# Kernel tuning notes

Measured on AMD Instinct MI355X. Metric: run time of the kernel, lower is better.

Reference implementation:

```python
import jax, jax.numpy as jnp
import numpy as np

B, L, D, N_NODE = 1024, 32, 128, 50000

def setup_inputs() -> dict:
    key = jax.random.key(0)
    ks = jax.random.split(key, 20)
    rn = lambda k, shape, s=0.05: (jax.random.normal(k, shape, jnp.float32) * s)
    return {
        "items": jax.random.randint(ks[0], (B, L), 0, N_NODE),
        "A_in": jax.random.uniform(ks[1], (B, L, L), jnp.float32),
        "A_out": jax.random.uniform(ks[2], (B, L, L), jnp.float32),
        "inter_item_emb": jax.random.normal(ks[3], (B, L, D), jnp.float32),
        "seq_len": jax.random.randint(ks[4], (B,), 1, L + 1),
        "emb_table": rn(ks[5], (N_NODE, D), 0.1),
        # GGNN propagation weights
        "W_in": rn(ks[6], (D, D)), "b_in": jnp.zeros((D,), jnp.float32),
        "W_out": rn(ks[7], (D, D)), "b_out": jnp.zeros((D,), jnp.float32),
        "W_a": rn(ks[8], (2 * D, 3 * D)),   # acts on concat(a_in, a_out)
        "U_h": rn(ks[9], (D, 3 * D)),       # acts on hidden state
        "b_gru": jnp.zeros((3 * D,), jnp.float32),
        # ItemFusing GRUCell (input=local/intra, hidden=global/inter)
        "Wi": rn(ks[10], (D, 3 * D)), "bi": jnp.zeros((3 * D,), jnp.float32),
        "Wh": rn(ks[11], (D, 3 * D)), "bh": jnp.zeros((3 * D,), jnp.float32),
        # get_final_s attention readout
        "W1": rn(ks[12], (D, D)), "b1": jnp.zeros((D,), jnp.float32),
        "W2": rn(ks[13], (D, D)), "b2": jnp.zeros((D,), jnp.float32),
        "wq": rn(ks[14], (D, 1)), "bq": jnp.zeros((1,), jnp.float32),
        "W3": rn(ks[15], (2 * D, D)), "b3": jnp.zeros((D,), jnp.float32),
    }

def _gru_gates(gi, gh, h_prev):
    # torch GRU(Cell) math: r,z,n gate order
    i_r, i_z, i_n = jnp.split(gi, 3, axis=-1)
    h_r, h_z, h_n = jnp.split(gh, 3, axis=-1)
    r = jax.nn.sigmoid(i_r + h_r)
    z = jax.nn.sigmoid(i_z + h_z)
    n = jnp.tanh(i_n + r * h_n)
    return (1.0 - z) * n + z * h_prev

def reference(items, A_in, A_out, inter_item_emb, seq_len, emb_table,
              W_in, b_in, W_out, b_out, W_a, U_h, b_gru,
              Wi, bi, Wh, bh, W1, b1, W2, b2, wq, bq, W3, b3):
    # --- embedding lookup: [B, L, D]
    h = emb_table[items]
    # --- GGNN propagation (1 step): adjacency matmul + GRU-gated update
    a_in = jnp.einsum('blm,bmd->bld', A_in, h @ W_in + b_in)
    a_out = jnp.einsum('blm,bmd->bld', A_out, h @ W_out + b_out)
    a = jnp.concatenate([a_in, a_out], axis=-1)          # [B, L, 2D]
    intra = _gru_gates(a @ W_a + b_gru, h @ U_h, h)       # [B, L, D]
    # --- ItemFusing: GRUCell(input=intra, hidden=inter)
    final = _gru_gates(intra @ Wi + bi, inter_item_emb @ Wh + bh, inter_item_emb)
    # --- get_final_s (session attention readout, padded/masked form)
    mask = (jnp.arange(L)[None, :] < seq_len[:, None]).astype(final.dtype)  # [B, L]
    v_n = final[jnp.arange(B), seq_len - 1]                                 # [B, D] last valid node
    gates = jax.nn.sigmoid((v_n @ W1 + b1)[:, None, :] + final @ W2 + b2)   # [B, L, D]
    alpha = gates @ wq + bq                                                 # [B, L, 1]
    s_g = jnp.sum(alpha * final * mask[:, :, None], axis=1)                 # [B, D]
    h_s = jnp.concatenate([v_n, s_g], axis=-1) @ W3 + b3                    # [B, D]
    # --- Embedding2Score (item_fusing branch): final_s @ emb.T
    scores = h_s @ emb_table.T                                              # [B, N_NODE]
    return scores
```

## Files before the change

### kernel.cpp

```cpp
#include <hip/hip_runtime.h>
#include <hip/hip_bf16.h>

#define L_SEQ 32
#define DIM 128
#define NN 50000

typedef __attribute__((ext_vector_type(8))) short bf16x8s;
typedef __attribute__((ext_vector_type(4))) float f32x4;

__device__ __forceinline__ float bf2f(short s){
    union{unsigned u; float f;} v; v.u = ((unsigned)(unsigned short)s) << 16; return v.f;
}
__device__ __forceinline__ short f2bf(float x){
    union{__hip_bfloat16 h; short s;} u; u.h = __float2bfloat16(x); return u.s;
}
__device__ __forceinline__ void ldf8(const float* p, float* w){
    const float4 a = *reinterpret_cast<const float4*>(p);
    const float4 b = *reinterpret_cast<const float4*>(p+4);
    w[0]=a.x; w[1]=a.y; w[2]=a.z; w[3]=a.w;
    w[4]=b.x; w[5]=b.y; w[6]=b.z; w[7]=b.w;
}
__device__ __forceinline__ void st8bf(short* dst, const float* v){
    union{ short s[8]; uint4 q; } u;
    #pragma unroll
    for (int i=0;i<8;++i) u.s[i] = f2bf(v[i]);
    *reinterpret_cast<uint4*>(dst) = u.q;
}
__device__ __forceinline__ bf16x8s cvt8(const float* v){
    union{ short s[8]; bf16x8s b; } u;
    #pragma unroll
    for (int i=0;i<8;++i) u.s[i] = f2bf(v[i]);
    return u.b;
}
__device__ __forceinline__ float sigmoidf(float x){ return 1.0f/(1.0f+__expf(-x)); }
__device__ __forceinline__ float tanh_fast(float x){
    x = fminf(fmaxf(x, -15.f), 15.f);
    float e = __expf(2.f*x);
    return (e-1.f)/(e+1.f);
}
__device__ __forceinline__ f32x4 mfma16(bf16x8s a, bf16x8s b, f32x4 c){
    return __builtin_amdgcn_mfma_f32_16x16x32_bf16(a, b, c, 0, 0, 0);
}

__global__ __launch_bounds__(256)
void transp_kernel(const float* __restrict__ W_in, const float* __restrict__ W_out,
                   const float* __restrict__ W_a,  const float* __restrict__ U_h,
                   const float* __restrict__ Wi,   const float* __restrict__ Wh,
                   const float* __restrict__ W1,   const float* __restrict__ W2,
                   const float* __restrict__ W3,   short* __restrict__ wt)
{
    int idx = blockIdx.x*256 + threadIdx.x;
    const float* src; int Rm1, lR, C, local, off;
    if      (idx < 16384) { src=W_in;  local=idx;        off=0;      Rm1=127; lR=7; C=128; }
    else if (idx < 32768) { src=W_out; local=idx-16384;  off=16384;  Rm1=127; lR=7; C=128; }
    else if (idx < 131072){ src=W_a;   local=idx-32768;  off=32768;  Rm1=255; lR=8; C=384; }
    else if (idx < 180224){ src=U_h;   local=idx-131072; off=131072; Rm1=127; lR=7; C=384; }
    else if (idx < 229376){ src=Wi;    local=idx-180224; off=180224; Rm1=127; lR=7; C=384; }
    else if (idx < 278528){ src=Wh;    local=idx-229376; off=229376; Rm1=127; lR=7; C=384; }
    else if (idx < 294912){ src=W1;    local=idx-278528; off=278528; Rm1=127; lR=7; C=128; }
    else if (idx < 311296){ src=W2;    local=idx-294912; off=294912; Rm1=127; lR=7; C=128; }
    else if (idx < 344064){ src=W3;    local=idx-311296; off=311296; Rm1=255; lR=8; C=128; }
    else return;
    int r = local & Rm1;
    int c = local >> lR;
    wt[off + local] = f2bf(src[r*C + c]);
}

__global__ __launch_bounds__(256)
void emb2bf(const float* __restrict__ emb, short* __restrict__ embf)
{
    const size_t idx = (size_t)(blockIdx.x*256 + threadIdx.x) * 8;
    float v[8]; ldf8(emb + idx, v);
    st8bf(embf + idx, v);
}

#define LDH 136
#define LDA 264
#define LDT 40

__global__ __launch_bounds__(256)
void graph_fused(const int* __restrict__ items,
                 const float* __restrict__ A_in, const float* __restrict__ A_out,
                 const float* __restrict__ inter,
                 const int* __restrict__ seq_len,
                 const float* __restrict__ emb,
                 const short* __restrict__ embf,
                 const float* __restrict__ b_in, const float* __restrict__ b_out,
                 const float* __restrict__ b_gru,
                 const float* __restrict__ bi, const float* __restrict__ bh,
                 const float* __restrict__ b1, const float* __restrict__ b2,
                 const float* __restrict__ wq, const float* __restrict__ bq,
                 const float* __restrict__ b3,
                 const short* __restrict__ wt,
                 short* __restrict__ hs_bf)
{
    const short* WinT  = wt + 0;
    const short* WoutT = wt + 16384;
    const short* WaT   = wt + 32768;
    const short* UhT   = wt + 131072;
    const short* WiT   = wt + 180224;
    const short* WhT   = wt + 229376;
    const short* W1T   = wt + 278528;
    const short* W2T   = wt + 294912;
    const short* W3T   = wt + 311296;

    __shared__ __align__(16) short s_h[32*LDH];
    __shared__ __align__(16) short s_a[32*LDA];
    __shared__ __align__(16) short s_r3[32*LDH];
    __shared__ __align__(16) short s_r4[2*32*LDH];

    short* s_Ain  = s_r3;
    short* s_Aout = s_r3 + 32*LDT;
    short* s_x    = s_r3;
    short* xT     = s_r4;
    short* s_int  = s_r4;
    short* s_fin  = s_r4 + 32*LDH;
    float* s_vn    = (float*)s_a;
    float* s_q1    = s_vn + 128;
    float* s_sg    = s_q1 + 128;
    float* s_red   = s_sg + 128;
    float* s_alpha = s_red + 256;

    const int b    = blockIdx.x;
    const int t    = threadIdx.x;
    const int wave = t >> 6;
    const int lane = t & 63;
    const int quad = lane >> 4;
    const int lc   = lane & 15;
    const int kq   = quad * 8;

    if (embf) {
        #pragma unroll
        for (int i=0;i<2;++i) {
            int c = t + i*256;
            int l = c >> 4, k = (c & 15) * 8;
            int it = items[b*L_SEQ + l];
            *reinterpret_cast<uint4*>(&s_h[l*LDH + k]) =
                *reinterpret_cast<const uint4*>(embf + (size_t)it*DIM + k);
        }
    } else {
        #pragma unroll
        for (int i=0;i<2;++i) {
            int c = t + i*256;
            int l = c >> 4, k = (c & 15) * 8;
            int it = items[b*L_SEQ + l];
            float v[8]; ldf8(emb + (size_t)it*DIM + k, v);
            st8bf(&s_h[l*LDH + k], v);
        }
    }
    {
        const int which = t >> 7;
        const int rem   = t & 127;
        const int l = rem >> 2, m = (rem & 3) * 8;
        const float* src = which ? A_out : A_in;
        float v[8]; ldf8(src + b*L_SEQ*L_SEQ + l*L_SEQ + m, v);
        st8bf((which ? s_Aout : s_Ain) + l*LDT + m, v);
    }
    __syncthreads();

    #pragma unroll
    for (int op = 0; op < 2; ++op) {
        const short* WT_ = op ? WoutT : WinT;
        #pragma unroll
        for (int p = 0; p < 2; ++p) {
            const int nt = wave*2 + p;
            const int n  = nt*16 + lc;
            const float bv = op ? b_out[n] : b_in[n];
            f32x4 acc0 = {bv,bv,bv,bv}, acc1 = {bv,bv,bv,bv};
            #pragma unroll
            for (int ks = 0; ks < 4; ++ks) {
                const int ko = ks*32 + kq;
                bf16x8s bb = *(const bf16x8s*)(WT_ + n*128 + ko);
                bf16x8s a0 = *(const bf16x8s*)(&s_h[(lc   )*LDH + ko]);
                bf16x8s a1 = *(const bf16x8s*)(&s_h[(16+lc)*LDH + ko]);
                acc0 = mfma16(a0, bb, acc0);
                acc1 = mfma16(a1, bb, acc1);
            }
            union{short s[4]; unsigned long long q;} u0, u1;
            #pragma unroll
            for (int i=0;i<4;++i){ u0.s[i]=f2bf(acc0[i]); u1.s[i]=f2bf(acc1[i]); }
            *(unsigned long long*)(&xT[n*LDT + 0  + quad*4]) = u0.q;
            *(unsigned long long*)(&xT[n*LDT + 16 + quad*4]) = u1.q;
        }
        __syncthreads();
        const short* Abuf = op ? s_Aout : s_Ain;
        #pragma unroll
        for (int u = 0; u < 4; ++u) {
            int unit = wave*4 + u;
            int nt = unit >> 1, m0 = (unit & 1)*16;
            bf16x8s a  = *(const bf16x8s*)(&Abuf[(m0+lc)*LDT + kq]);
            bf16x8s bb = *(const bf16x8s*)(&xT[(nt*16+lc)*LDT + kq]);
            f32x4 acc = {0.f,0.f,0.f,0.f};
            acc = mfma16(a, bb, acc);
            #pragma unroll
            for (int i=0;i<4;++i)
                s_a[(m0+quad*4+i)*LDA + op*128 + nt*16 + lc] = f2bf(acc[i]);
        }
        __syncthreads();
    }

    #pragma unroll
    for (int i=0;i<2;++i) {
        int c = t + i*256;
        int l = c >> 4, k = (c & 15) * 8;
        float v[8]; ldf8(inter + ((size_t)b*L_SEQ + l)*DIM + k, v);
        st8bf(&s_int[l*LDH + k], v);
    }

    #pragma unroll
    for (int g = wave; g < 8; g += 4) {
        const int n = g*16 + lc;
        const float vr = b_gru[n], vz = b_gru[128+n], vn2 = b_gru[256+n];
        f32x4 ar[2], az[2], an[2], pr[2], pz[2], pn[2];
        #pragma unroll
        for (int m=0;m<2;++m){
            ar[m]=(f32x4){vr,vr,vr,vr}; az[m]=(f32x4){vz,vz,vz,vz}; an[m]=(f32x4){vn2,vn2,vn2,vn2};
            pr[m]=(f32x4){0,0,0,0}; pz[m]=pr[m]; pn[m]=pr[m];
        }
        #pragma unroll
        for (int ks=0; ks<8; ++ks) {
            const int ko = ks*32 + kq;
            bf16x8s br = *(const bf16x8s*)(WaT + (n      )*256 + ko);
            bf16x8s bz = *(const bf16x8s*)(WaT + (n + 128)*256 + ko);
            bf16x8s bn = *(const bf16x8s*)(WaT + (n + 256)*256 + ko);
            #pragma unroll
            for (int m=0;m<2;++m){
                bf16x8s a = *(const bf16x8s*)(&s_a[(m*16+lc)*LDA + ko]);
                ar[m]=mfma16(a,br,ar[m]); az[m]=mfma16(a,bz,az[m]); an[m]=mfma16(a,bn,an[m]);
            }
        }
        #pragma unroll
        for (int ks=0; ks<4; ++ks) {
            const int ko = ks*32 + kq;
            bf16x8s br = *(const bf16x8s*)(UhT + (n      )*128 + ko);
            bf16x8s bz = *(const bf16x8s*)(UhT + (n + 128)*128 + ko);
            bf16x8s bn = *(const bf16x8s*)(UhT + (n + 256)*128 + ko);
            #pragma unroll
            for (int m=0;m<2;++m){
                bf16x8s a = *(const bf16x8s*)(&s_h[(m*16+lc)*LDH + ko]);
                pr[m]=mfma16(a,br,pr[m]); pz[m]=mfma16(a,bz,pz[m]); pn[m]=mfma16(a,bn,pn[m]);
            }
        }
        #pragma unroll
        for (int m=0;m<2;++m)
        #pragma unroll
        for (int i=0;i<4;++i){
            const int row = m*16 + quad*4 + i;
            float hp = bf2f(s_h[row*LDH + n]);
            float r  = sigmoidf(ar[m][i] + pr[m][i]);
            float z  = sigmoidf(az[m][i] + pz[m][i]);
            float nn = tanh_fast(an[m][i] + r*pn[m][i]);
            s_x[row*LDH + n] = f2bf((1.f - z)*nn + z*hp);
        }
    }
    __syncthreads();

    #pragma unroll
    for (int g = wave; g < 8; g += 4) {
        const int n = g*16 + lc;
        const float vir = bi[n], viz = bi[128+n], vin = bi[256+n];
        const float vhr = bh[n], vhz = bh[128+n], vhn = bh[256+n];
        f32x4 ar[2], az[2], an[2], pr[2], pz[2], pn[2];
        #pragma unroll
        for (int m=0;m<2;++m){
            ar[m]=(f32x4){vir,vir,vir,vir}; az[m]=(f32x4){viz,viz,viz,viz}; an[m]=(f32x4){vin,vin,vin,vin};
            pr[m]=(f32x4){vhr,vhr,vhr,vhr}; pz[m]=(f32x4){vhz,vhz,vhz,vhz}; pn[m]=(f32x4){vhn,vhn,vhn,vhn};
        }
        #pragma unroll
        for (int ks=0; ks<4; ++ks) {
            const int ko = ks*32 + kq;
            bf16x8s br = *(const bf16x8s*)(WiT + (n      )*128 + ko);
            bf16x8s bz = *(const bf16x8s*)(WiT + (n + 128)*128 + ko);
            bf16x8s bn = *(const bf16x8s*)(WiT + (n + 256)*128 + ko);
            #pragma unroll
            for (int m=0;m<2;++m){
                bf16x8s a = *(const bf16x8s*)(&s_x[(m*16+lc)*LDH + ko]);
                ar[m]=mfma16(a,br,ar[m]); az[m]=mfma16(a,bz,az[m]); an[m]=mfma16(a,bn,an[m]);
            }
        }
        #pragma unroll
        for (int ks=0; ks<4; ++ks) {
            const int ko = ks*32 + kq;
            bf16x8s br = *(const bf16x8s*)(WhT + (n      )*128 + ko);
            bf16x8s bz = *(const bf16x8s*)(WhT + (n + 128)*128 + ko);
            bf16x8s bn = *(const bf16x8s*)(WhT + (n + 256)*128 + ko);
            #pragma unroll
            for (int m=0;m<2;++m){
                bf16x8s a = *(const bf16x8s*)(&s_int[(m*16+lc)*LDH + ko]);
                pr[m]=mfma16(a,br,pr[m]); pz[m]=mfma16(a,bz,pz[m]); pn[m]=mfma16(a,bn,pn[m]);
            }
        }
        #pragma unroll
        for (int m=0;m<2;++m)
        #pragma unroll
        for (int i=0;i<4;++i){
            const int row = m*16 + quad*4 + i;
            float hp = bf2f(s_int[row*LDH + n]);
            float r  = sigmoidf(ar[m][i] + pr[m][i]);
            float z  = sigmoidf(az[m][i] + pz[m][i]);
            float nn = tanh_fast(an[m][i] + r*pn[m][i]);
            s_fin[row*LDH + n] = f2bf((1.f - z)*nn + z*hp);
        }
    }
    __syncthreads();

    const int slen = seq_len[b];
    if (t < DIM) s_vn[t] = bf2f(s_fin[(slen-1)*LDH + t]);
    __syncthreads();
    if (t < DIM) {
        float acc = b1[t] + b2[t];
        #pragma unroll
        for (int k8=0; k8<16; ++k8) {
            union{ uint4 q; short s[8]; } u;
            u.q = *reinterpret_cast<const uint4*>(W1T + t*128 + k8*8);
            #pragma unroll
            for (int u2=0;u2<8;++u2) acc += s_vn[k8*8+u2]*bf2f(u.s[u2]);
        }
        s_q1[t] = acc;
    }
    __syncthreads();
    #pragma unroll
    for (int tl = wave; tl < 16; tl += 4) {
        const int m0 = (tl & 1)*16, nt = tl >> 1;
        const int n  = nt*16 + lc;
        f32x4 acc = {0.f,0.f,0.f,0.f};
        #pragma unroll
        for (int ks=0; ks<4; ++ks) {
            const int ko = ks*32 + kq;
            bf16x8s a  = *(const bf16x8s*)(&s_fin[(m0+lc)*LDH + ko]);
            bf16x8s bb = *(const bf16x8s*)(W2T + n*128 + ko);
            acc = mfma16(a, bb, acc);
        }
        const float qb  = s_q1[n];
        const float wqv = wq[n];
        float p[4];
        #pragma unroll
        for (int i=0;i<4;++i) p[i] = sigmoidf(acc[i] + qb) * wqv;
        #pragma unroll
        for (int off=1; off<16; off<<=1) {
            #pragma unroll
            for (int i=0;i<4;++i) p[i] += __shfl_xor(p[i], off);
        }
        if (lc == 0) {
            #pragma unroll
            for (int i=0;i<4;++i) s_red[(m0+quad*4+i)*8 + nt] = p[i];
        }
    }
    __syncthreads();
    if (t < L_SEQ) {
        float al = bq[0];
        #pragma unroll
        for (int u=0;u<8;++u) al += s_red[t*8+u];
        s_alpha[t] = (t < slen) ? al : 0.f;
    }
    __syncthreads();
    if (t < DIM) {
        float sg = 0.f;
        #pragma unroll
        for (int l=0;l<L_SEQ;++l) sg += s_alpha[l]*bf2f(s_fin[l*LDH + t]);
        s_sg[t] = sg;
    }
    __syncthreads();
    if (t < DIM) {
        float acc = b3[t];
        #pragma unroll
        for (int k8=0; k8<16; ++k8) {
            union{ uint4 q; short s[8]; } u;
            u.q = *reinterpret_cast<const uint4*>(W3T + t*256 + k8*8);
            #pragma unroll
            for (int u2=0;u2<8;++u2) acc += s_vn[k8*8+u2]*bf2f(u.s[u2]);
        }
        #pragma unroll
        for (int k8=0; k8<16; ++k8) {
            union{ uint4 q; short s[8]; } u;
            u.q = *reinterpret_cast<const uint4*>(W3T + t*256 + 128 + k8*8);
            #pragma unroll
            for (int u2=0;u2<8;++u2) acc += s_sg[k8*8+u2]*bf2f(u.s[u2]);
        }
        hs_bf[b*DIM + t] = f2bf(acc);
    }
}

__global__ __launch_bounds__(256)
void scores_bf(const short* __restrict__ hs, const short* __restrict__ embf,
               float* __restrict__ out)
{
    const int t    = threadIdx.x;
    const int wave = t >> 6;
    const int lane = t & 63;
    const int quad = lane >> 4;
    const int lc   = lane & 15;
    const int kq   = quad * 8;
    const int n0   = blockIdx.x * 64;
    const int mb   = blockIdx.y * 256 + wave*64;

    bf16x8s hf[4][4];
    #pragma unroll
    for (int mi=0; mi<4; ++mi)
        #pragma unroll
        for (int ks=0; ks<4; ++ks)
            hf[mi][ks] = *(const bf16x8s*)(hs + (size_t)(mb + mi*16 + lc)*DIM + ks*32 + kq);

    #pragma unroll
    for (int nt=0; nt<4; ++nt) {
        const int nr  = n0 + nt*16 + lc;
        const int nld = nr < NN ? nr : NN-1;
        bf16x8s ef[4];
        #pragma unroll
        for (int ks=0; ks<4; ++ks)
            ef[ks] = *(const bf16x8s*)(embf + (size_t)nld*DIM + ks*32 + kq);
        const int nbase = n0 + nt*16 + quad*4;
        #pragma unroll
        for (int mi=0; mi<4; ++mi) {
            f32x4 acc = {0.f,0.f,0.f,0.f};
            #pragma unroll
            for (int ks=0; ks<4; ++ks) acc = mfma16(ef[ks], hf[mi][ks], acc);
            if (nbase < NN) {
                __builtin_nontemporal_store(acc,
                    reinterpret_cast<f32x4*>(&out[(size_t)(mb + mi*16 + lc)*NN + nbase]));
            }
        }
    }
}

__global__ __launch_bounds__(256)
void scores_kernel(const short* __restrict__ hs, const float* __restrict__ emb,
                   float* __restrict__ out)
{
    const int t    = threadIdx.x;
    const int wave = t >> 6;
    const int lane = t & 63;
    const int quad = lane >> 4;
    const int lc   = lane & 15;
    const int kq   = quad * 8;
    const int n0   = blockIdx.x * 64;
    const int m0   = blockIdx.y * 64 + wave*16;

    bf16x8s af[4];
    #pragma unroll
    for (int ks=0; ks<4; ++ks)
        af[ks] = *(const bf16x8s*)(hs + (size_t)(m0 + lc)*DIM + ks*32 + kq);

    #pragma unroll
    for (int nt=0; nt<4; ++nt) {
        const int nabs = n0 + nt*16 + lc;
        const int nld  = nabs < NN ? nabs : NN-1;
        f32x4 acc = {0.f,0.f,0.f,0.f};
        #pragma unroll
        for (int ks=0; ks<4; ++ks) {
            float v[8]; ldf8(emb + (size_t)nld*DIM + ks*32 + kq, v);
            acc = mfma16(af[ks], cvt8(v), acc);
        }
        if (nabs < NN) {
            #pragma unroll
            for (int i=0;i<4;++i)
                out[(size_t)(m0 + quad*4 + i)*NN + nabs] = acc[i];
        }
    }
}

extern "C" void kernel_launch(void* const* d_in, const int* in_sizes, int n_in,
                              void* d_out, int out_size, void* d_ws, size_t ws_size,
                              hipStream_t stream)
{
    const int*   items   = (const int*)  d_in[0];
    const float* A_in    = (const float*)d_in[1];
    const float* A_out   = (const float*)d_in[2];
    const float* inter   = (const float*)d_in[3];
    const int*   seq_len = (const int*)  d_in[4];
    const float* emb     = (const float*)d_in[5];
    const float* W_in = (const float*)d_in[6],  *b_in  = (const float*)d_in[7];
    const float* W_out= (const float*)d_in[8],  *b_out = (const float*)d_in[9];
    const float* W_a  = (const float*)d_in[10], *U_h   = (const float*)d_in[11];
    const float* b_gru= (const float*)d_in[12];
    const float* Wi   = (const float*)d_in[13], *bi    = (const float*)d_in[14];
    const float* Wh   = (const float*)d_in[15], *bh    = (const float*)d_in[16];
    const float* W1   = (const float*)d_in[17], *b1    = (const float*)d_in[18];
    const float* W2   = (const float*)d_in[19], *b2    = (const float*)d_in[20];
    const float* wq   = (const float*)d_in[21], *bq    = (const float*)d_in[22];
    const float* W3   = (const float*)d_in[23], *b3    = (const float*)d_in[24];
    float* out = (float*)d_out;
    short* hs_bf = (short*)d_ws;
    short* wt    = (short*)((char*)d_ws + 262144);
    short* embf  = (short*)((char*)d_ws + 1048576);

    const size_t need_bf = 1048576 + (size_t)NN*DIM*2;
    const bool use_bf = (ws_size >= need_bf);

    transp_kernel<<<1344, 256, 0, stream>>>(W_in, W_out, W_a, U_h, Wi, Wh, W1, W2, W3, wt);
    if (use_bf)
        emb2bf<<<3125, 256, 0, stream>>>(emb, embf);
    graph_fused<<<1024, 256, 0, stream>>>(items, A_in, A_out, inter, seq_len, emb,
        use_bf ? embf : (const short*)nullptr,
        b_in, b_out, b_gru, bi, bh, b1, b2, wq, bq, b3, wt, hs_bf);
    if (use_bf)
        scores_bf<<<dim3(782, 4), 256, 0, stream>>>(hs_bf, embf, out);
    else
        scores_kernel<<<dim3(782, 16), 256, 0, stream>>>(hs_bf, emb, out);
}
```

Before: 407.0 us.

## Merge prep kernels, pre-convert inter embeddings to bf16, restructure scores tiling

Folds the weight transpose and the embedding-table bf16 conversion into one prep launch, which now also converts inter_item_emb to bf16 so graph_fused can prefetch it early as raw 16-byte loads. The scores kernel now keeps a 64-row tile of the embedding table in registers and loops over all 1024 batch rows per block, so each embedding row is read once instead of once per grid-y tile. The grid shrinks from 782x4 to 782x1 blocks, which lowers parallelism per launch and moves more serial work into each wave. It also needs a larger workspace, and the bf16 path is skipped if the workspace is too small.

```diff
diff --git a/kernel.cpp b/kernel.cpp
--- a/kernel.cpp
+++ b/kernel.cpp
@@ -43,35 +43,40 @@
 }
 
 __global__ __launch_bounds__(256)
-void transp_kernel(const float* __restrict__ W_in, const float* __restrict__ W_out,
-                   const float* __restrict__ W_a,  const float* __restrict__ U_h,
-                   const float* __restrict__ Wi,   const float* __restrict__ Wh,
-                   const float* __restrict__ W1,   const float* __restrict__ W2,
-                   const float* __restrict__ W3,   short* __restrict__ wt)
+void prep_kernel(const float* __restrict__ W_in, const float* __restrict__ W_out,
+                 const float* __restrict__ W_a,  const float* __restrict__ U_h,
+                 const float* __restrict__ Wi,   const float* __restrict__ Wh,
+                 const float* __restrict__ W1,   const float* __restrict__ W2,
+                 const float* __restrict__ W3,   short* __restrict__ wt,
+                 const float* __restrict__ emb,  short* __restrict__ embf,
+                 const float* __restrict__ inter, short* __restrict__ intf)
 {
-    int idx = blockIdx.x*256 + threadIdx.x;
-    const float* src; int Rm1, lR, C, local, off;
-    if      (idx < 16384) { src=W_in;  local=idx;        off=0;      Rm1=127; lR=7; C=128; }
-    else if (idx < 32768) { src=W_out; local=idx-16384;  off=16384;  Rm1=127; lR=7; C=128; }
-    else if (idx < 131072){ src=W_a;   local=idx-32768;  off=32768;  Rm1=255; lR=8; C=384; }
-    else if (idx < 180224){ src=U_h;   local=idx-131072; off=131072; Rm1=127; lR=7; C=384; }
-    else if (idx < 229376){ src=Wi;    local=idx-180224; off=180224; Rm1=127; lR=7; C=384; }
-    else if (idx < 278528){ src=Wh;    local=idx-229376; off=229376; Rm1=127; lR=7; C=384; }
-    else if (idx < 294912){ src=W1;    local=idx-278528; off=278528; Rm1=127; lR=7; C=128; }
-    else if (idx < 311296){ src=W2;    local=idx-294912; off=294912; Rm1=127; lR=7; C=128; }
-    else if (idx < 344064){ src=W3;    local=idx-311296; off=311296; Rm1=255; lR=8; C=128; }
-    else return;
-    int r = local & Rm1;
-    int c = local >> lR;
-    wt[off + local] = f2bf(src[r*C + c]);
-}
-
-__global__ __launch_bounds__(256)
-void emb2bf(const float* __restrict__ emb, short* __restrict__ embf)
-{
-    const size_t idx = (size_t)(blockIdx.x*256 + threadIdx.x) * 8;
-    float v[8]; ldf8(emb + idx, v);
-    st8bf(embf + idx, v);
+    const int blk = blockIdx.x;
+    if (blk < 1344) {
+        int idx = blk*256 + threadIdx.x;
+        const float* src; int Rm1, lR, C, local, off;
+        if      (idx < 16384) { src=W_in;  local=idx;        off=0;      Rm1=127; lR=7; C=128; }
+        else if (idx < 32768) { src=W_out; local=idx-16384;  off=16384;  Rm1=127; lR=7; C=128; }
+        else if (idx < 131072){ src=W_a;   local=idx-32768;  off=32768;  Rm1=255; lR=8; C=384; }
+        else if (idx < 180224){ src=U_h;   local=idx-131072; off=131072; Rm1=127; lR=7; C=384; }
+        else if (idx < 229376){ src=Wi;    local=idx-180224; off=180224; Rm1=127; lR=7; C=384; }
+        else if (idx < 278528){ src=Wh;    local=idx-229376; off=229376; Rm1=127; lR=7; C=384; }
+        else if (idx < 294912){ src=W1;    local=idx-278528; off=278528; Rm1=127; lR=7; C=128; }
+        else if (idx < 311296){ src=W2;    local=idx-294912; off=294912; Rm1=127; lR=7; C=128; }
+        else if (idx < 344064){ src=W3;    local=idx-311296; off=311296; Rm1=255; lR=8; C=128; }
+        else return;
+        int r = local & Rm1;
+        int c = local >> lR;
+        wt[off + local] = f2bf(src[r*C + c]);
+    } else if (blk < 4469) {
+        const size_t idx = ((size_t)(blk-1344)*256 + threadIdx.x) * 8;
+        float v[8]; ldf8(emb + idx, v);
+        st8bf(embf + idx, v);
+    } else {
+        const size_t idx = ((size_t)(blk-4469)*256 + threadIdx.x) * 8;
+        float v[8]; ldf8(inter + idx, v);
+        st8bf(intf + idx, v);
+    }
 }
 
 #define LDH 136
@@ -85,6 +90,7 @@
                  const int* __restrict__ seq_len,
                  const float* __restrict__ emb,
                  const short* __restrict__ embf,
+                 const short* __restrict__ intf,
                  const float* __restrict__ b_in, const float* __restrict__ b_out,
                  const float* __restrict__ b_gru,
                  const float* __restrict__ bi, const float* __restrict__ bh,
@@ -129,7 +135,13 @@
     const int lc   = lane & 15;
     const int kq   = quad * 8;
 
-    if (embf) {
+    uint4 pre_i[2];
+    const bool fast = (embf != nullptr);
+    if (fast) {
+        #pragma unroll
+        for (int i=0;i<2;++i)
+            pre_i[i] = *reinterpret_cast<const uint4*>(
+                intf + (size_t)b*L_SEQ*DIM + (size_t)(t + i*256)*8);
         #pragma unroll
         for (int i=0;i<2;++i) {
             int c = t + i*256;
@@ -199,12 +211,21 @@
         __syncthreads();
     }
 
-    #pragma unroll
-    for (int i=0;i<2;++i) {
-        int c = t + i*256;
-        int l = c >> 4, k = (c & 15) * 8;
-        float v[8]; ldf8(inter + ((size_t)b*L_SEQ + l)*DIM + k, v);
-        st8bf(&s_int[l*LDH + k], v);
+    if (fast) {
+        #pragma unroll
+        for (int i=0;i<2;++i) {
+            int c = t + i*256;
+            int l = c >> 4, k = (c & 15) * 8;
+            *reinterpret_cast<uint4*>(&s_int[l*LDH + k]) = pre_i[i];
+        }
+    } else {
+        #pragma unroll
+        for (int i=0;i<2;++i) {
+            int c = t + i*256;
+            int l = c >> 4, k = (c & 15) * 8;
+            float v[8]; ldf8(inter + ((size_t)b*L_SEQ + l)*DIM + k, v);
+            st8bf(&s_int[l*LDH + k], v);
+        }
     }
 
     #pragma unroll
@@ -392,32 +413,33 @@
     const int lc   = lane & 15;
     const int kq   = quad * 8;
     const int n0   = blockIdx.x * 64;
-    const int mb   = blockIdx.y * 256 + wave*64;
-
-    bf16x8s hf[4][4];
-    #pragma unroll
-    for (int mi=0; mi<4; ++mi)
-        #pragma unroll
-        for (int ks=0; ks<4; ++ks)
-            hf[mi][ks] = *(const bf16x8s*)(hs + (size_t)(mb + mi*16 + lc)*DIM + ks*32 + kq);
-
+
+    bf16x8s ef[4][4];
     #pragma unroll
     for (int nt=0; nt<4; ++nt) {
         const int nr  = n0 + nt*16 + lc;
         const int nld = nr < NN ? nr : NN-1;
-        bf16x8s ef[4];
         #pragma unroll
         for (int ks=0; ks<4; ++ks)
-            ef[ks] = *(const bf16x8s*)(embf + (size_t)nld*DIM + ks*32 + kq);
-        const int nbase = n0 + nt*16 + quad*4;
-        #pragma unroll
-        for (int mi=0; mi<4; ++mi) {
+            ef[nt][ks] = *(const bf16x8s*)(embf + (size_t)nld*DIM + ks*32 + kq);
+    }
+
+    const int mbase = wave * 256;
+    for (int mt = 0; mt < 16; ++mt) {
+        const int mrow = mbase + mt*16 + lc;
+        bf16x8s hf[4];
+        #pragma unroll
+        for (int ks=0; ks<4; ++ks)
+            hf[ks] = *(const bf16x8s*)(hs + (size_t)mrow*DIM + ks*32 + kq);
+        #pragma unroll
+        for (int nt=0; nt<4; ++nt) {
+            const int nbase = n0 + nt*16 + quad*4;
             f32x4 acc = {0.f,0.f,0.f,0.f};
             #pragma unroll
-            for (int ks=0; ks<4; ++ks) acc = mfma16(ef[ks], hf[mi][ks], acc);
+            for (int ks=0; ks<4; ++ks) acc = mfma16(ef[nt][ks], hf[ks], acc);
             if (nbase < NN) {
                 __builtin_nontemporal_store(acc,
-                    reinterpret_cast<f32x4*>(&out[(size_t)(mb + mi*16 + lc)*NN + nbase]));
+                    reinterpret_cast<f32x4*>(&out[(size_t)mrow*NN + nbase]));
             }
         }
     }
@@ -483,18 +505,19 @@
     short* hs_bf = (short*)d_ws;
     short* wt    = (short*)((char*)d_ws + 262144);
     short* embf  = (short*)((char*)d_ws + 1048576);
-
-    const size_t need_bf = 1048576 + (size_t)NN*DIM*2;
+    short* intf  = (short*)((char*)d_ws + 1048576 + 12800000);
+
+    const size_t need_bf = 1048576 + 12800000 + 8388608;
     const bool use_bf = (ws_size >= need_bf);
 
-    transp_kernel<<<1344, 256, 0, stream>>>(W_in, W_out, W_a, U_h, Wi, Wh, W1, W2, W3, wt);
-    if (use_bf)
-        emb2bf<<<3125, 256, 0, stream>>>(emb, embf);
+    prep_kernel<<<use_bf ? 6517 : 1344, 256, 0, stream>>>(
+        W_in, W_out, W_a, U_h, Wi, Wh, W1, W2, W3, wt, emb, embf, inter, intf);
     graph_fused<<<1024, 256, 0, stream>>>(items, A_in, A_out, inter, seq_len, emb,
         use_bf ? embf : (const short*)nullptr,
+        use_bf ? intf : (const short*)nullptr,
         b_in, b_out, b_gru, bi, bh, b1, b2, wq, bq, b3, wt, hs_bf);
     if (use_bf)
-        scores_bf<<<dim3(782, 4), 256, 0, stream>>>(hs_bf, embf, out);
+        scores_bf<<<dim3(782, 1), 256, 0, stream>>>(hs_bf, embf, out);
     else
         scores_kernel<<<dim3(782, 16), 256, 0, stream>>>(hs_bf, emb, out);
 }
```

Measured after the change: 421.2 us. +3.5%, slower.
